# Performance work log

Measured on AMD Instinct MI355X. Metric: run time of the kernel, lower is better.

## Reference

```python
import jax, jax.numpy as jnp
import numpy as np

BETA = 0.25


def setup_inputs() -> dict:
    key = jax.random.key(0)
    k1, k2 = jax.random.split(key)
    B, T, D, K = 16, 4096, 256, 4096
    z_e = jax.random.normal(k1, (B, T, D), dtype=jnp.float32)
    # emulate uniform(-1/K, 1/K) init but any values work for correctness
    codebook = jax.random.uniform(k2, (K, D), dtype=jnp.float32,
                                  minval=-1.0 / K, maxval=1.0 / K)
    return {"z_e": z_e, "codebook": codebook}


def reference(z_e, codebook):
    D = codebook.shape[1]
    z_flat = z_e.reshape(-1, D)                                  # [N, D]
    # squared L2 distances: ||z||^2 + ||e||^2 - 2 z.e
    z_norm = jnp.sum(z_flat ** 2, axis=1, keepdims=True)          # [N, 1]
    e_norm = jnp.sum(codebook ** 2, axis=1)                       # [K]
    dist = z_norm + e_norm - 2.0 * jnp.matmul(z_flat, codebook.T) # [N, K]
    idx_flat = jnp.argmin(dist, axis=1)                           # [N]
    idx = idx_flat.reshape(z_e.shape[:-1])                        # [B, T]
    z_q = codebook[idx]                                           # [B, T, D]
    # commitment loss: beta * mse(stop_grad(z_q), z_e)
    loss = BETA * jnp.mean((jax.lax.stop_gradient(z_q) - z_e) ** 2)
    # straight-through estimator
    z_q_st = z_e + jax.lax.stop_gradient(z_q - z_e)
    return z_q_st, idx, loss
```

## Files before the change

kernel.cpp:

```cpp
#include <hip/hip_runtime.h>
#include <cfloat>

#define NROWS 65536
#define DIM   256
#define KCB   4096

#define EPS_WIN  1.8e-4f
#define CAND_CAP 16
#define SROWS    64

typedef __attribute__((ext_vector_type(8))) short short8;
typedef __attribute__((ext_vector_type(4))) float f32x4;

__device__ inline unsigned short f2bf(float x) {
  unsigned int u = __float_as_uint(x);
  return (unsigned short)((u + 0x7fffu + ((u >> 16) & 1u)) >> 16);
}

__global__ void prep_norms_kernel(const float* __restrict__ z, const float* __restrict__ cb,
                                  unsigned short* __restrict__ zh, unsigned short* __restrict__ eh,
                                  float* __restrict__ znorm, float* __restrict__ enorm) {
  const int r    = blockIdx.x * 4 + (threadIdx.x >> 6);
  const int lane = threadIdx.x & 63;
  const float* src; unsigned short* dst; float* nrm; int row;
  if (r < NROWS) { src = z;  dst = zh; nrm = znorm; row = r; }
  else           { src = cb; dst = eh; nrm = enorm; row = r - NROWS; }
  const float4 v = ((const float4*)(src + (size_t)row * DIM))[lane];
  union { unsigned short us[4]; uint2 u2; } o;
  o.us[0] = f2bf(v.x); o.us[1] = f2bf(v.y); o.us[2] = f2bf(v.z); o.us[3] = f2bf(v.w);
  *(uint2*)(dst + (size_t)row * DIM + lane * 4) = o.u2;
  float s = v.x * v.x + v.y * v.y + v.z * v.z + v.w * v.w;
  #pragma unroll
  for (int off = 32; off > 0; off >>= 1) s += __shfl_down(s, off);
  if (lane == 0) nrm[row] = s;
}

__launch_bounds__(256, 3)
__global__ void screen_kernel(const unsigned short* __restrict__ zh,
                              const unsigned short* __restrict__ eh,
                              const float* __restrict__ enorm,
                              unsigned int* __restrict__ counts,
                              unsigned short* __restrict__ cands) {
  __shared__ __align__(16) unsigned short a_s[8][SROWS][32];
  __shared__ __align__(16) unsigned short b_s[2][128][32];
  __shared__ unsigned int cnt_s[SROWS];
  __shared__ unsigned short cand_s[SROWS * CAND_CAP];

  const int tid = threadIdx.x;
  const int wv  = tid >> 6;
  const int ln  = tid & 63;
  const int l15 = ln & 15;
  const int lg  = ln >> 4;
  const int rbase = blockIdx.x * SROWS;

  if (tid < SROWS) cnt_s[tid] = 0u;

  {
    const unsigned short* abase = zh + (size_t)rbase * DIM;
    unsigned short* aflat = &a_s[0][0][0];
    #pragma unroll
    for (int i = 0; i < 8; ++i) {
      const int G  = i * 256 + tid;
      const int dc = G >> 8, rem = G & 255;
      const int c  = rem >> 2, sw = rem & 3;
      const int s4 = sw ^ ((c >> 1) & 3);
      __builtin_amdgcn_global_load_lds(
          (const uint4*)(abase + (size_t)c * 256 + dc * 32 + s4 * 8),
          (uint4*)(aflat + (size_t)G * 8), 16, 0, 0);
    }
    unsigned short* b0 = &b_s[0][0][0];
    #pragma unroll
    for (int i = 0; i < 2; ++i) {
      const int G  = i * 256 + tid;
      const int c  = G >> 2, sw = G & 3;
      const int s4 = sw ^ ((c >> 1) & 3);
      __builtin_amdgcn_global_load_lds(
          (const uint4*)(eh + (size_t)c * 256 + s4 * 8),
          (uint4*)(b0 + (size_t)G * 8), 16, 0, 0);
    }
  }
  __syncthreads();

  const int ar = l15;
  const int arow = wv * 16 + ar;
  const int asl = lg ^ ((arow >> 1) & 3);

  float rm[4];
  #pragma unroll
  for (int q = 0; q < 4; ++q) rm[q] = FLT_MAX;

  int cur = 0;

  #pragma unroll 1
  for (int kt = 0; kt < KCB / 128; ++kt) {
    const int kcb0 = kt * 128;

    f32x4 acc[8];
    #pragma unroll
    for (int fc = 0; fc < 8; ++fc) acc[fc] = (f32x4){0.f, 0.f, 0.f, 0.f};

    #pragma unroll 1
    for (int dc = 0; dc < 8; ++dc) {
      {
        const int t   = (kt * 8 + dc + 1) & 255;
        const int nkt = t >> 3, ndc = t & 7;
        unsigned short* bn = &b_s[cur ^ 1][0][0];
        #pragma unroll
        for (int i = 0; i < 2; ++i) {
          const int G  = i * 256 + tid;
          const int c  = G >> 2, sw = G & 3;
          const int s4 = sw ^ ((c >> 1) & 3);
          __builtin_amdgcn_global_load_lds(
              (const uint4*)(eh + (size_t)(nkt * 128 + c) * 256 + ndc * 32 + s4 * 8),
              (uint4*)(bn + (size_t)G * 8), 16, 0, 0);
        }
      }

      const short8 af = *(const short8*)(&a_s[dc][arow][asl * 8]);
      short8 bf[8];
      #pragma unroll
      for (int fc = 0; fc < 8; ++fc) {
        const int c  = fc * 16 + l15;
        const int sw = lg ^ ((c >> 1) & 3);
        bf[fc] = *(const short8*)(&b_s[cur][c][sw * 8]);
      }
      #pragma unroll
      for (int fc = 0; fc < 8; ++fc)
        acc[fc] = __builtin_amdgcn_mfma_f32_16x16x32_bf16(af, bf[fc], acc[fc], 0, 0, 0);

      __syncthreads();
      cur ^= 1;
    }

    float en_[8];
    #pragma unroll
    for (int fc = 0; fc < 8; ++fc) en_[fc] = enorm[kcb0 + fc * 16 + l15];

    float tm[4];
    #pragma unroll
    for (int q = 0; q < 4; ++q) tm[q] = FLT_MAX;

    #pragma unroll
    for (int fc = 0; fc < 8; ++fc)
      #pragma unroll
      for (int q = 0; q < 4; ++q) {
        const float d_ = fmaf(-2.0f, acc[fc][q], en_[fc]);
        tm[q] = fminf(tm[q], d_);
      }

    float gmin = FLT_MAX;
    #pragma unroll
    for (int q = 0; q < 4; ++q) {
      float v = tm[q];
      v = fminf(v, __shfl_xor(v, 1));
      v = fminf(v, __shfl_xor(v, 2));
      v = fminf(v, __shfl_xor(v, 4));
      v = fminf(v, __shfl_xor(v, 8));
      const float m = fminf(rm[q], v);
      rm[q] = m;
      gmin = fminf(gmin, tm[q] - m);
    }

    if (__any(gmin <= EPS_WIN)) {
      #pragma unroll
      for (int fc = 0; fc < 8; ++fc)
        #pragma unroll
        for (int q = 0; q < 4; ++q) {
          const float d_ = fmaf(-2.0f, acc[fc][q], en_[fc]);
          if (d_ <= rm[q] + EPS_WIN) {
            const int rl = wv * 16 + lg * 4 + q;
            const unsigned int pos = atomicAdd(&cnt_s[rl], 1u);
            if (pos < CAND_CAP)
              cand_s[rl * CAND_CAP + pos] =
                  (unsigned short)(kcb0 + fc * 16 + l15);
          }
        }
    }
  }

  __syncthreads();
  if (tid < SROWS) counts[rbase + tid] = cnt_s[tid];
  for (int i = tid; i < SROWS * CAND_CAP; i += 256)
    cands[(size_t)rbase * CAND_CAP + i] = cand_s[i];
}

__global__ void rescore_kernel(const float* __restrict__ z, const float* __restrict__ cb,
                               const float* __restrict__ znorm, const float* __restrict__ enorm,
                               const unsigned int* __restrict__ counts,
                               const unsigned short* __restrict__ cands,
                               float* __restrict__ out_zq, float* __restrict__ out_idx,
                               float* __restrict__ partials) {
  const int gw  = (blockIdx.x * 256 + threadIdx.x) >> 6;
  const int ln  = threadIdx.x & 63;
  const int row = gw * 4 + (ln >> 4);
  const int ci  = ln & 15;
  const unsigned int cnt = counts[row];
  if (cnt > CAND_CAP) return;

  const int active = ci < (int)cnt;
  const int k = active ? (int)cands[(size_t)row * CAND_CAP + ci] : 0;
  const float4* zr4 = (const float4*)(z  + (size_t)row * DIM);
  const float4* er4 = (const float4*)(cb + (size_t)k   * DIM);
  float ax = 0.f, ay = 0.f, az = 0.f, aw = 0.f;
  #pragma unroll 4
  for (int d = 0; d < DIM / 4; ++d) {
    const float4 zv = zr4[d], ev = er4[d];
    ax = fmaf(zv.x, ev.x, ax); ay = fmaf(zv.y, ev.y, ay);
    az = fmaf(zv.z, ev.z, az); aw = fmaf(zv.w, ev.w, aw);
  }
  const float dot = (ax + ay) + (az + aw);
  const float dist = fmaf(-2.0f, dot, znorm[row] + enorm[k]);
  float bv = active ? dist : FLT_MAX;
  int   bk = active ? k : 0x7fffffff;
  #pragma unroll
  for (int off = 1; off < 16; off <<= 1) {
    const float ov = __shfl_xor(bv, off);
    const int   ok = __shfl_xor(bk, off);
    if (ov < bv || (ov == bv && ok < bk)) { bv = ov; bk = ok; }
  }
  const float4* br4 = (const float4*)(cb + (size_t)bk * DIM);
  float4* o4 = (float4*)(out_zq + (size_t)row * DIM);
  float sq = 0.0f;
  #pragma unroll
  for (int t = 0; t < 4; ++t) {
    const int p = ci + 16 * t;
    const float4 zv = zr4[p], ev = br4[p];
    float4 st;
    const float dx = ev.x - zv.x, dy = ev.y - zv.y, dz = ev.z - zv.z, dw = ev.w - zv.w;
    st.x = zv.x + dx; st.y = zv.y + dy; st.z = zv.z + dz; st.w = zv.w + dw;
    o4[p] = st;
    sq += dx * dx + dy * dy + dz * dz + dw * dw;
  }
  #pragma unroll
  for (int off = 1; off < 16; off <<= 1) sq += __shfl_xor(sq, off);
  if (ci == 0) { out_idx[row] = (float)bk; partials[row] = sq; }
}

__global__ void fallback_kernel(const float* __restrict__ z, const float* __restrict__ cb,
                                const float* __restrict__ znorm, const float* __restrict__ enorm,
                                const unsigned int* __restrict__ counts,
                                float* __restrict__ out_zq, float* __restrict__ out_idx,
                                float* __restrict__ partials) {
  __shared__ float bd_s[256];
  __shared__ int   bk_s[256];
  const int tid = threadIdx.x;
  for (int row = blockIdx.x; row < NROWS; row += gridDim.x) {
    if (counts[row] <= CAND_CAP) continue;
    const float zn = znorm[row];
    const float* zr = z + (size_t)row * DIM;
    float bv = FLT_MAX; int bk = 0x7fffffff;
    for (int k = tid; k < KCB; k += 256) {
      const float* er = cb + (size_t)k * DIM;
      float acc = 0.0f;
      #pragma unroll 8
      for (int d = 0; d < DIM; ++d) acc = fmaf(zr[d], er[d], acc);
      const float dist = fmaf(-2.0f, acc, zn + enorm[k]);
      if (dist < bv || (dist == bv && k < bk)) { bv = dist; bk = k; }
    }
    bd_s[tid] = bv; bk_s[tid] = bk;
    __syncthreads();
    for (int s = 128; s > 0; s >>= 1) {
      if (tid < s) {
        const float ov = bd_s[tid + s]; const int ok = bk_s[tid + s];
        if (ov < bd_s[tid] || (ov == bd_s[tid] && ok < bk_s[tid])) {
          bd_s[tid] = ov; bk_s[tid] = ok;
        }
      }
      __syncthreads();
    }
    const int kb = bk_s[0];
    const float zv = zr[tid];
    const float ev = cb[(size_t)kb * DIM + tid];
    const float dd = ev - zv;
    out_zq[(size_t)row * DIM + tid] = zv + dd;
    if (tid == 0) out_idx[row] = (float)kb;
    __syncthreads();
    bd_s[tid] = dd * dd;
    __syncthreads();
    for (int s = 128; s > 0; s >>= 1) {
      if (tid < s) bd_s[tid] += bd_s[tid + s];
      __syncthreads();
    }
    if (tid == 0) partials[row] = bd_s[0];
    __syncthreads();
  }
}

__global__ void loss_kernel(const float* __restrict__ partials, int n,
                            float* __restrict__ out_loss) {
  float s = 0.0f;
  for (int i = threadIdx.x; i < n; i += 256) s += partials[i];
  #pragma unroll
  for (int off = 32; off > 0; off >>= 1) s += __shfl_down(s, off);
  __shared__ float ps[4];
  if ((threadIdx.x & 63) == 0) ps[threadIdx.x >> 6] = s;
  __syncthreads();
  if (threadIdx.x == 0)
    *out_loss = 0.25f * (((ps[0] + ps[1]) + (ps[2] + ps[3])) *
                         (1.0f / (float)((size_t)NROWS * DIM)));
}

__global__ void norms_kernel(const float* __restrict__ x, float* __restrict__ out) {
  const int row  = blockIdx.x * 4 + (threadIdx.x >> 6);
  const int lane = threadIdx.x & 63;
  const float4 v = ((const float4*)(x + (size_t)row * DIM))[lane];
  float s = v.x * v.x + v.y * v.y + v.z * v.z + v.w * v.w;
  #pragma unroll
  for (int off = 32; off > 0; off >>= 1) s += __shfl_down(s, off);
  if (lane == 0) out[row] = s;
}

#define BM 128
#define BK 128
#define BD 32
#define LSTR 36
__launch_bounds__(256, 2)
__global__ void argmin_kernel(const float* __restrict__ z,
                              const float* __restrict__ cb,
                              const float* __restrict__ znorm,
                              const float* __restrict__ enorm,
                              int* __restrict__ idx_out) {
  __shared__ float z_s[BM * LSTR];
  __shared__ float e_s[BK * LSTR];
  __shared__ float zn_s[BM];
  const int tid = threadIdx.x;
  const int tx = tid & 15;
  const int ty = tid >> 4;
  const int rbase = blockIdx.x * BM;
  if (tid < BM) zn_s[tid] = znorm[rbase + tid];
  float bestv[8]; int besti[8];
  #pragma unroll
  for (int i = 0; i < 8; ++i) { bestv[i] = FLT_MAX; besti[i] = 0; }
  for (int kc = 0; kc < KCB; kc += BK) {
    float acc[8][8];
    #pragma unroll
    for (int i = 0; i < 8; ++i)
      #pragma unroll
      for (int j = 0; j < 8; ++j) acc[i][j] = 0.0f;
    for (int dc = 0; dc < DIM; dc += BD) {
      __syncthreads();
      #pragma unroll
      for (int p = 0; p < 4; ++p) {
        const int el = p * 256 + tid;
        const int r  = el >> 3;
        const int c4 = (el & 7) * 4;
        *(float4*)(&z_s[r * LSTR + c4]) =
            *(const float4*)(z + (size_t)(rbase + r) * DIM + dc + c4);
        *(float4*)(&e_s[r * LSTR + c4]) =
            *(const float4*)(cb + (size_t)(kc + r) * DIM + dc + c4);
      }
      __syncthreads();
      #pragma unroll 1
      for (int dd = 0; dd < BD; dd += 4) {
        float4 b[8];
        #pragma unroll
        for (int j = 0; j < 8; ++j)
          b[j] = *(const float4*)(&e_s[(tx + 16 * j) * LSTR + dd]);
        #pragma unroll
        for (int i = 0; i < 8; ++i) {
          const float4 a = *(const float4*)(&z_s[(ty + 16 * i) * LSTR + dd]);
          #pragma unroll
          for (int j = 0; j < 8; ++j)
            acc[i][j] += a.x * b[j].x + a.y * b[j].y + a.z * b[j].z + a.w * b[j].w;
        }
      }
    }
    float en[8];
    #pragma unroll
    for (int j = 0; j < 8; ++j) en[j] = enorm[kc + tx + 16 * j];
    #pragma unroll
    for (int i = 0; i < 8; ++i) {
      const float zn = zn_s[ty + 16 * i];
      #pragma unroll
      for (int j = 0; j < 8; ++j) {
        const float t1 = zn + en[j];
        const float dist = t1 - 2.0f * acc[i][j];
        const int k = kc + tx + 16 * j;
        if (dist < bestv[i]) { bestv[i] = dist; besti[i] = k; }
      }
    }
  }
  #pragma unroll
  for (int i = 0; i < 8; ++i) {
    float lv = bestv[i]; int li = besti[i];
    #pragma unroll
    for (int off = 1; off < 16; off <<= 1) {
      const float ov = __shfl_xor(lv, off);
      const int   oi = __shfl_xor(li, off);
      if (ov < lv || (ov == lv && oi < li)) { lv = ov; li = oi; }
    }
    if (tx == 0) idx_out[rbase + ty + 16 * i] = li;
  }
}

__global__ void gather_kernel(const float* __restrict__ z,
                              const float* __restrict__ cb,
                              const int* __restrict__ idx,
                              float* __restrict__ out_zq,
                              float* __restrict__ out_idx,
                              float* __restrict__ partials) {
  const int row  = blockIdx.x * 4 + (threadIdx.x >> 6);
  const int lane = threadIdx.x & 63;
  const int k = idx[row];
  const float4 zv = ((const float4*)(z  + (size_t)row * DIM))[lane];
  const float4 ev = ((const float4*)(cb + (size_t)k   * DIM))[lane];
  float4 d, st;
  d.x = ev.x - zv.x; d.y = ev.y - zv.y; d.z = ev.z - zv.z; d.w = ev.w - zv.w;
  st.x = zv.x + d.x; st.y = zv.y + d.y; st.z = zv.z + d.z; st.w = zv.w + d.w;
  ((float4*)(out_zq + (size_t)row * DIM))[lane] = st;
  if (lane == 0) out_idx[row] = (float)k;
  float s = d.x * d.x + d.y * d.y + d.z * d.z + d.w * d.w;
  #pragma unroll
  for (int off = 32; off > 0; off >>= 1) s += __shfl_down(s, off);
  __shared__ float ps[4];
  if (lane == 0) ps[threadIdx.x >> 6] = s;
  __syncthreads();
  if (threadIdx.x == 0)
    partials[blockIdx.x] = (ps[0] + ps[1]) + (ps[2] + ps[3]);
}

extern "C" void kernel_launch(void* const* d_in, const int* in_sizes, int n_in,
                              void* d_out, int out_size, void* d_ws, size_t ws_size,
                              hipStream_t stream) {
  const float* z  = (const float*)d_in[0];
  const float* cb = (const float*)d_in[1];

  float* out_zq   = (float*)d_out;
  float* out_idx  = out_zq + (size_t)NROWS * DIM;
  float* out_loss = out_idx + NROWS;

  char* w = (char*)d_ws;
  unsigned short* zh    = (unsigned short*)(w);
  unsigned short* eh    = (unsigned short*)(w + 33554432);
  float* enorm          = (float*)(w + 35651584);
  float* znorm          = (float*)(w + 35667968);
  unsigned int* counts  = (unsigned int*)(w + 36192256);
  unsigned short* cands = (unsigned short*)(w + 36454400);
  float* partials       = (float*)(w + 38551552);
  const size_t NEED = 38813696;

  if (ws_size >= NEED) {
    hipLaunchKernelGGL(prep_norms_kernel, dim3((NROWS + KCB) / 4), dim3(256), 0, stream,
                       z, cb, zh, eh, znorm, enorm);
    hipLaunchKernelGGL(screen_kernel, dim3(NROWS / SROWS), dim3(256), 0, stream,
                       zh, eh, enorm, counts, cands);
    hipLaunchKernelGGL(rescore_kernel, dim3(NROWS / 16), dim3(256), 0, stream,
                       z, cb, znorm, enorm, counts, cands, out_zq, out_idx, partials);
    hipLaunchKernelGGL(fallback_kernel, dim3(256), dim3(256), 0, stream,
                       z, cb, znorm, enorm, counts, out_zq, out_idx, partials);
    hipLaunchKernelGGL(loss_kernel, dim3(1), dim3(256), 0, stream,
                       partials, NROWS, out_loss);
  } else {
    float* ws         = (float*)d_ws;
    float* enorm_l    = ws;
    float* znorm_l    = ws + KCB;
    int*   idx_l      = (int*)(ws + KCB + NROWS);
    float* partials_l = ws + KCB + 2 * NROWS;
    hipLaunchKernelGGL(norms_kernel, dim3(KCB / 4), dim3(256), 0, stream, cb, enorm_l);
    hipLaunchKernelGGL(norms_kernel, dim3(NROWS / 4), dim3(256), 0, stream, z, znorm_l);
    hipLaunchKernelGGL(argmin_kernel, dim3(NROWS / BM), dim3(256), 0, stream,
                       z, cb, znorm_l, enorm_l, idx_l);
    hipLaunchKernelGGL(gather_kernel, dim3(NROWS / 4), dim3(256), 0, stream,
                       z, cb, idx_l, out_zq, out_idx, partials_l);
    hipLaunchKernelGGL(loss_kernel, dim3(1), dim3(256), 0, stream,
                       partials_l, NROWS / 4, out_loss);
  }
}
```

Before: 547.2 us.

## Switch screen kernel to 32x32x16 MFMA with 256-code tiles split across waves

Reworks the screening GEMM so each wave computes all 64 rows against its own 64-code slice of a 256-wide codebook tile, using 32x32x16 bf16 MFMAs instead of 16x16x32 ones. A-fragment LDS reads are now shared across two column fragments, which raises operand reuse per LDS load, and each codebook tile is fetched in bigger chunks. The per-row running minimum now needs a cross-wave reduction through shared memory with two extra barriers per tile. Occupancy hint drops from 3 to 2 blocks per CU because of the larger accumulator and running-min register state.

After: 570.3 us. 1.04x slower.

```diff
diff --git a/kernel.cpp b/kernel.cpp
--- a/kernel.cpp
+++ b/kernel.cpp
@@ -8,9 +8,11 @@
 #define EPS_WIN  1.8e-4f
 #define CAND_CAP 16
 #define SROWS    64
-
-typedef __attribute__((ext_vector_type(8))) short short8;
-typedef __attribute__((ext_vector_type(4))) float f32x4;
+#define KTW      256
+
+typedef __attribute__((ext_vector_type(8)))  short short8;
+typedef __attribute__((ext_vector_type(4)))  float f32x4;
+typedef __attribute__((ext_vector_type(16))) float f32x16;
 
 __device__ inline unsigned short f2bf(float x) {
   unsigned int u = __float_as_uint(x);
@@ -35,25 +37,28 @@
   if (lane == 0) nrm[row] = s;
 }
 
-__launch_bounds__(256, 3)
+__launch_bounds__(256, 2)
 __global__ void screen_kernel(const unsigned short* __restrict__ zh,
                               const unsigned short* __restrict__ eh,
                               const float* __restrict__ enorm,
                               unsigned int* __restrict__ counts,
                               unsigned short* __restrict__ cands) {
   __shared__ __align__(16) unsigned short a_s[8][SROWS][32];
-  __shared__ __align__(16) unsigned short b_s[2][128][32];
+  __shared__ __align__(16) unsigned short b_s[2][KTW][32];
+  __shared__ __align__(16) float tilemin_s[4][SROWS];
   __shared__ unsigned int cnt_s[SROWS];
   __shared__ unsigned short cand_s[SROWS * CAND_CAP];
 
   const int tid = threadIdx.x;
   const int wv  = tid >> 6;
   const int ln  = tid & 63;
-  const int l15 = ln & 15;
-  const int lg  = ln >> 4;
+  const int l31 = ln & 31;
+  const int hi  = ln >> 5;
   const int rbase = blockIdx.x * SROWS;
 
   if (tid < SROWS) cnt_s[tid] = 0u;
+
+  unsigned short* bflat = &b_s[0][0][0];
 
   {
     const unsigned short* abase = zh + (size_t)rbase * DIM;
@@ -68,117 +73,152 @@
           (const uint4*)(abase + (size_t)c * 256 + dc * 32 + s4 * 8),
           (uint4*)(aflat + (size_t)G * 8), 16, 0, 0);
     }
-    unsigned short* b0 = &b_s[0][0][0];
-    #pragma unroll
-    for (int i = 0; i < 2; ++i) {
+    #pragma unroll
+    for (int i = 0; i < 4; ++i) {
       const int G  = i * 256 + tid;
       const int c  = G >> 2, sw = G & 3;
       const int s4 = sw ^ ((c >> 1) & 3);
       __builtin_amdgcn_global_load_lds(
           (const uint4*)(eh + (size_t)c * 256 + s4 * 8),
-          (uint4*)(b0 + (size_t)G * 8), 16, 0, 0);
+          (uint4*)(bflat + (size_t)G * 8), 16, 0, 0);
     }
   }
   __syncthreads();
 
-  const int ar = l15;
-  const int arow = wv * 16 + ar;
-  const int asl = lg ^ ((arow >> 1) & 3);
-
-  float rm[4];
-  #pragma unroll
-  for (int q = 0; q < 4; ++q) rm[q] = FLT_MAX;
+  const int axor = (l31 >> 1) & 3;
+  float rm[2][16];
+  #pragma unroll
+  for (int fr = 0; fr < 2; ++fr)
+    #pragma unroll
+    for (int rg = 0; rg < 16; ++rg) rm[fr][rg] = FLT_MAX;
 
   int cur = 0;
 
   #pragma unroll 1
-  for (int kt = 0; kt < KCB / 128; ++kt) {
-    const int kcb0 = kt * 128;
-
-    f32x4 acc[8];
-    #pragma unroll
-    for (int fc = 0; fc < 8; ++fc) acc[fc] = (f32x4){0.f, 0.f, 0.f, 0.f};
+  for (int kt = 0; kt < KCB / KTW; ++kt) {
+    const int kcb0 = kt * KTW;
+
+    f32x16 acc[2][2];
+    #pragma unroll
+    for (int fr = 0; fr < 2; ++fr)
+      #pragma unroll
+      for (int fc = 0; fc < 2; ++fc)
+        #pragma unroll
+        for (int rg = 0; rg < 16; ++rg) acc[fr][fc][rg] = 0.0f;
 
     #pragma unroll 1
-    for (int dc = 0; dc < 8; ++dc) {
+    for (int ch = 0; ch < 8; ++ch) {
       {
-        const int t   = (kt * 8 + dc + 1) & 255;
-        const int nkt = t >> 3, ndc = t & 7;
-        unsigned short* bn = &b_s[cur ^ 1][0][0];
-        #pragma unroll
-        for (int i = 0; i < 2; ++i) {
+        const int t   = (kt * 8 + ch + 1) & 127;
+        const int nkt = t >> 3, nch = t & 7;
+        unsigned short* bn = bflat + (size_t)(cur ^ 1) * (KTW * 32);
+        #pragma unroll
+        for (int i = 0; i < 4; ++i) {
           const int G  = i * 256 + tid;
           const int c  = G >> 2, sw = G & 3;
           const int s4 = sw ^ ((c >> 1) & 3);
           __builtin_amdgcn_global_load_lds(
-              (const uint4*)(eh + (size_t)(nkt * 128 + c) * 256 + ndc * 32 + s4 * 8),
+              (const uint4*)(eh + (size_t)(nkt * KTW + c) * 256 + nch * 32 + s4 * 8),
               (uint4*)(bn + (size_t)G * 8), 16, 0, 0);
         }
       }
 
-      const short8 af = *(const short8*)(&a_s[dc][arow][asl * 8]);
-      short8 bf[8];
-      #pragma unroll
-      for (int fc = 0; fc < 8; ++fc) {
-        const int c  = fc * 16 + l15;
-        const int sw = lg ^ ((c >> 1) & 3);
-        bf[fc] = *(const short8*)(&b_s[cur][c][sw * 8]);
-      }
-      #pragma unroll
-      for (int fc = 0; fc < 8; ++fc)
-        acc[fc] = __builtin_amdgcn_mfma_f32_16x16x32_bf16(af, bf[fc], acc[fc], 0, 0, 0);
+      #pragma unroll
+      for (int s = 0; s < 2; ++s) {
+        const int sl = (s * 2 + hi) ^ axor;
+        short8 af[2], bf[2];
+        #pragma unroll
+        for (int fr = 0; fr < 2; ++fr)
+          af[fr] = *(const short8*)(&a_s[ch][fr * 32 + l31][sl * 8]);
+        #pragma unroll
+        for (int fc = 0; fc < 2; ++fc)
+          bf[fc] = *(const short8*)(&b_s[cur][wv * 64 + fc * 32 + l31][sl * 8]);
+        #pragma unroll
+        for (int fr = 0; fr < 2; ++fr)
+          #pragma unroll
+          for (int fc = 0; fc < 2; ++fc)
+            acc[fr][fc] = __builtin_amdgcn_mfma_f32_32x32x16_bf16(
+                af[fr], bf[fc], acc[fr][fc], 0, 0, 0);
+      }
 
       __syncthreads();
       cur ^= 1;
     }
 
-    float en_[8];
-    #pragma unroll
-    for (int fc = 0; fc < 8; ++fc) en_[fc] = enorm[kcb0 + fc * 16 + l15];
-
-    float tm[4];
-    #pragma unroll
-    for (int q = 0; q < 4; ++q) tm[q] = FLT_MAX;
-
-    #pragma unroll
-    for (int fc = 0; fc < 8; ++fc)
-      #pragma unroll
-      for (int q = 0; q < 4; ++q) {
-        const float d_ = fmaf(-2.0f, acc[fc][q], en_[fc]);
-        tm[q] = fminf(tm[q], d_);
-      }
+    const float en0 = enorm[kcb0 + wv * 64 + l31];
+    const float en1 = enorm[kcb0 + wv * 64 + 32 + l31];
+
+    float tm[2][16];
+    #pragma unroll
+    for (int fr = 0; fr < 2; ++fr)
+      #pragma unroll
+      for (int rg = 0; rg < 16; ++rg) {
+        const float d0 = fmaf(-2.0f, acc[fr][0][rg], en0);
+        const float d1 = fmaf(-2.0f, acc[fr][1][rg], en1);
+        float v = fminf(d0, d1);
+        v = fminf(v, __shfl_xor(v, 1));
+        v = fminf(v, __shfl_xor(v, 2));
+        v = fminf(v, __shfl_xor(v, 4));
+        v = fminf(v, __shfl_xor(v, 8));
+        v = fminf(v, __shfl_xor(v, 16));
+        tm[fr][rg] = v;
+      }
+
+    if (l31 == 0) {
+      #pragma unroll
+      for (int fr = 0; fr < 2; ++fr)
+        #pragma unroll
+        for (int rg = 0; rg < 16; ++rg)
+          tilemin_s[wv][fr * 32 + (rg & 3) + 8 * (rg >> 2) + 4 * hi] = tm[fr][rg];
+    }
+    __syncthreads();
+
+    if (tid < SROWS)
+      tilemin_s[0][tid] = fminf(fminf(tilemin_s[0][tid], tilemin_s[1][tid]),
+                                fminf(tilemin_s[2][tid], tilemin_s[3][tid]));
+    __syncthreads();
 
     float gmin = FLT_MAX;
     #pragma unroll
-    for (int q = 0; q < 4; ++q) {
-      float v = tm[q];
-      v = fminf(v, __shfl_xor(v, 1));
-      v = fminf(v, __shfl_xor(v, 2));
-      v = fminf(v, __shfl_xor(v, 4));
-      v = fminf(v, __shfl_xor(v, 8));
-      const float m = fminf(rm[q], v);
-      rm[q] = m;
-      gmin = fminf(gmin, tm[q] - m);
-    }
+    for (int fr = 0; fr < 2; ++fr)
+      #pragma unroll
+      for (int g = 0; g < 4; ++g) {
+        const f32x4 cv = *(const f32x4*)(&tilemin_s[0][fr * 32 + g * 8 + 4 * hi]);
+        #pragma unroll
+        for (int j = 0; j < 4; ++j) {
+          const int rg = g * 4 + j;
+          const float m = fminf(rm[fr][rg], cv[j]);
+          rm[fr][rg] = m;
+          gmin = fminf(gmin, tm[fr][rg] - m);
+        }
+      }
 
     if (__any(gmin <= EPS_WIN)) {
       #pragma unroll
-      for (int fc = 0; fc < 8; ++fc)
-        #pragma unroll
-        for (int q = 0; q < 4; ++q) {
-          const float d_ = fmaf(-2.0f, acc[fc][q], en_[fc]);
-          if (d_ <= rm[q] + EPS_WIN) {
-            const int rl = wv * 16 + lg * 4 + q;
-            const unsigned int pos = atomicAdd(&cnt_s[rl], 1u);
+      for (int fr = 0; fr < 2; ++fr)
+        #pragma unroll
+        for (int rg = 0; rg < 16; ++rg) {
+          const float th = rm[fr][rg] + EPS_WIN;
+          const int row = fr * 32 + (rg & 3) + 8 * (rg >> 2) + 4 * hi;
+          const float d0 = fmaf(-2.0f, acc[fr][0][rg], en0);
+          if (d0 <= th) {
+            const unsigned int pos = atomicAdd(&cnt_s[row], 1u);
             if (pos < CAND_CAP)
-              cand_s[rl * CAND_CAP + pos] =
-                  (unsigned short)(kcb0 + fc * 16 + l15);
+              cand_s[row * CAND_CAP + pos] =
+                  (unsigned short)(kcb0 + wv * 64 + l31);
+          }
+          const float d1 = fmaf(-2.0f, acc[fr][1][rg], en1);
+          if (d1 <= th) {
+            const unsigned int pos = atomicAdd(&cnt_s[row], 1u);
+            if (pos < CAND_CAP)
+              cand_s[row * CAND_CAP + pos] =
+                  (unsigned short)(kcb0 + wv * 64 + 32 + l31);
           }
         }
     }
-  }
-
-  __syncthreads();
+    __syncthreads();
+  }
+
   if (tid < SROWS) counts[rbase + tid] = cnt_s[tid];
   for (int i = tid; i < SROWS * CAND_CAP; i += 256)
     cands[(size_t)rbase * CAND_CAP + i] = cand_s[i];
```
